# Kernel optimization log

Measured on AMD Instinct MI355X. Metric: run time of the kernel, lower is better.

The kernel has to match this reference:

```python
import jax, jax.numpy as jnp
import numpy as np

N_PER_TYPE = 32000
N = 3 * N_PER_TYPE          # 96000 nodes
E = N * 16                  # 1,536,000 edges
H, D = 4, 8                 # num_heads, out_dim per head; hidden = 32
IN_DIMS = [128, 64, 32]
NEG_SLOPE = 0.2


def setup_inputs() -> dict:
    key = jax.random.key(0)
    ks = jax.random.split(key, 16)
    inp = {}
    # per-type raw features
    inp['x0'] = jax.random.normal(ks[0], (N_PER_TYPE, IN_DIMS[0]), jnp.float32)
    inp['x1'] = jax.random.normal(ks[1], (N_PER_TYPE, IN_DIMS[1]), jnp.float32)
    inp['x2'] = jax.random.normal(ks[2], (N_PER_TYPE, IN_DIMS[2]), jnp.float32)
    # per-type linear params (fc_list), scaled like kaiming-ish init
    inp['W0'] = jax.random.normal(ks[3], (IN_DIMS[0], H * D), jnp.float32) / np.sqrt(IN_DIMS[0])
    inp['b0'] = jnp.zeros((H * D,), jnp.float32)
    inp['W1'] = jax.random.normal(ks[4], (IN_DIMS[1], H * D), jnp.float32) / np.sqrt(IN_DIMS[1])
    inp['b1'] = jnp.zeros((H * D,), jnp.float32)
    inp['W2'] = jax.random.normal(ks[5], (IN_DIMS[2], H * D), jnp.float32) / np.sqrt(IN_DIMS[2])
    inp['b2'] = jnp.zeros((H * D,), jnp.float32)
    # GAT attention vectors a_l, a_r per head
    inp['attn_l'] = jax.random.normal(ks[6], (H, D), jnp.float32) / np.sqrt(D)
    inp['attn_r'] = jax.random.normal(ks[7], (H, D), jnp.float32) / np.sqrt(D)
    # node types laid out in contiguous blocks -> fixed-size index sets
    inp['type_mask'] = jnp.repeat(jnp.arange(3, dtype=jnp.int32), N_PER_TYPE)
    inp['idx0'] = jnp.arange(0, N_PER_TYPE, dtype=jnp.int32)
    inp['idx1'] = jnp.arange(N_PER_TYPE, 2 * N_PER_TYPE, dtype=jnp.int32)
    inp['idx2'] = jnp.arange(2 * N_PER_TYPE, 3 * N_PER_TYPE, dtype=jnp.int32)
    # random edge list
    inp['src'] = jax.random.randint(ks[8], (E,), 0, N, jnp.int32)
    inp['dst'] = jax.random.randint(ks[9], (E,), 0, N, jnp.int32)
    return inp


def reference(x0, x1, x2, W0, b0, W1, b1, W2, b2, attn_l, attn_r,
              idx0, idx1, idx2, src, dst, type_mask):
    # ---- type-masked per-type linear embed scattered into dense buffer ----
    t = jnp.zeros((N, H * D), x0.dtype)
    t = t.at[idx0].set(x0 @ W0 + b0)
    t = t.at[idx1].set(x1 @ W1 + b1)
    t = t.at[idx2].set(x2 @ W2 + b2)
    # (feat_drop is identity in eval mode)
    h = t.reshape(N, H, D)
    # ---- multi-head GAT attention ----
    el = jnp.einsum('nhd,hd->nh', h, attn_l)   # [N,H]
    er = jnp.einsum('nhd,hd->nh', h, attn_r)   # [N,H]
    e = jax.nn.leaky_relu(el[src] + er[dst], NEG_SLOPE)  # [E,H]
    # segment softmax over incoming edges of each dst node
    m = jax.ops.segment_max(e, dst, num_segments=N)      # [N,H]
    m = jnp.where(jnp.isfinite(m), m, 0.0)               # guard isolated nodes
    ex = jnp.exp(e - m[dst])                             # [E,H]
    s = jax.ops.segment_sum(ex, dst, num_segments=N)     # [N,H]
    alpha = ex / (s[dst] + 1e-9)                         # [E,H]
    # message aggregation
    msg = alpha[:, :, None] * h[src]                     # [E,H,D]
    out = jax.ops.segment_sum(msg, dst, num_segments=N)  # [N,H,D]
    # concat heads + ELU (standard intermediate-layer GAT activation)
    return jax.nn.elu(out).reshape(N, H * D)
```

## Files before the change

kernel.cpp:

```cpp
#include <hip/hip_runtime.h>
#include <hip/hip_bf16.h>
#include <math.h>

#define N_PER_TYPE 32000
#define NN (3 * N_PER_TYPE)
#define EDGES (NN * 16)
#define NHEAD 4
#define HD 32
#define NEG 0.2f
#define BINS 256
#define NPB (NN / BINS)
#define TILES 256
#define TPE (EDGES / TILES)
#define MAXBIN 8192
#define NB_EMBED 1500

typedef __attribute__((ext_vector_type(8))) short bf16x8;
typedef __attribute__((ext_vector_type(4))) float f32x4;

__device__ __forceinline__ unsigned packbf(float a, float b) {
    __hip_bfloat162 t = __float22bfloat162_rn(make_float2(a, b));
    return *reinterpret_cast<unsigned*>(&t);
}

__global__ __launch_bounds__(256) void embed_p1_kernel(
    const float* __restrict__ x0, const float* __restrict__ x1, const float* __restrict__ x2,
    const float* __restrict__ W0, const float* __restrict__ b0,
    const float* __restrict__ W1, const float* __restrict__ b1,
    const float* __restrict__ W2, const float* __restrict__ b2,
    const float* __restrict__ attn_l, const float* __restrict__ attn_r,
    __hip_bfloat16* __restrict__ h16, float* __restrict__ el, float* __restrict__ er,
    const int* __restrict__ dst, int* __restrict__ counts)
{
    int blk = blockIdx.x;
    int tid = threadIdx.x;

    if (blk >= NB_EMBED) {
        __shared__ int hist[BINS];
        int tile = blk - NB_EMBED;
        for (int i = tid; i < BINS; i += 256) hist[i] = 0;
        __syncthreads();
        int e0 = tile * TPE;
        for (int t = e0 + tid; t < e0 + TPE; t += 256)
            atomicAdd(&hist[dst[t] / NPB], 1);
        __syncthreads();
        for (int i = tid; i < BINS; i += 256) counts[tile * BINS + i] = hist[i];
        return;
    }

    __shared__ unsigned Wb[2048];
    __shared__ float hepi[64][33];

    int type = blk / 500;
    int nb = blk % 500;

    const float* x; const float* W; const float* bia; int in_dim;
    if (type == 0)      { x = x0; W = W0; bia = b0; in_dim = 128; }
    else if (type == 1) { x = x1; W = W1; bia = b1; in_dim = 64; }
    else                { x = x2; W = W2; bia = b2; in_dim = 32; }
    int KS = in_dim >> 5;

    int ndw = KS << 9;
    for (int i = tid; i < ndw; i += 256) {
        int d = i & 3, l = (i >> 2) & 63, sn = i >> 8;
        int s = sn >> 1, n = sn & 1;
        int k = (s << 5) + ((l >> 4) << 3) + (d << 1);
        int col = (n << 4) + (l & 15);
        Wb[i] = packbf(W[k * 32 + col], W[(k + 1) * 32 + col]);
    }
    __syncthreads();

    int wave = tid >> 6, lane = tid & 63;
    int node_l0 = wave * 16 + (lane & 15);
    const float* xrow = x + (size_t)(nb * 64 + node_l0) * in_dim;
    int kg = lane >> 4;

    f32x4 acc0 = {0.f, 0.f, 0.f, 0.f};
    f32x4 acc1 = {0.f, 0.f, 0.f, 0.f};

    for (int s = 0; s < KS; ++s) {
        int k0 = (s << 5) + (kg << 3);
        float4 xa = *(const float4*)(xrow + k0);
        float4 xb = *(const float4*)(xrow + k0 + 4);
        union { unsigned u[4]; bf16x8 v; } a;
        a.u[0] = packbf(xa.x, xa.y);
        a.u[1] = packbf(xa.z, xa.w);
        a.u[2] = packbf(xb.x, xb.y);
        a.u[3] = packbf(xb.z, xb.w);
        bf16x8 bfr0 = *(const bf16x8*)&Wb[((s * 2 + 0) * 64 + lane) * 4];
        bf16x8 bfr1 = *(const bf16x8*)&Wb[((s * 2 + 1) * 64 + lane) * 4];
        acc0 = __builtin_amdgcn_mfma_f32_16x16x32_bf16(a.v, bfr0, acc0, 0, 0, 0);
        acc1 = __builtin_amdgcn_mfma_f32_16x16x32_bf16(a.v, bfr1, acc1, 0, 0, 0);
    }

    int hrow = wave * 16 + ((lane >> 4) << 2);
    int hcol = lane & 15;
    #pragma unroll
    for (int r = 0; r < 4; ++r) {
        hepi[hrow + r][hcol]      = acc0[r];
        hepi[hrow + r][hcol + 16] = acc1[r];
    }
    __syncthreads();

    int node_e = tid >> 2, head = tid & 3;
    int node = blk * 64 + node_e;
    float4 al = *(const float4*)(attn_l + head * 8);
    float4 al2 = *(const float4*)(attn_l + head * 8 + 4);
    float4 ar = *(const float4*)(attn_r + head * 8);
    float4 ar2 = *(const float4*)(attn_r + head * 8 + 4);
    float hv[8];
    #pragma unroll
    for (int i = 0; i < 8; ++i) hv[i] = hepi[node_e][head * 8 + i] + bia[head * 8 + i];

    float elv = hv[0]*al.x + hv[1]*al.y + hv[2]*al.z + hv[3]*al.w
              + hv[4]*al2.x + hv[5]*al2.y + hv[6]*al2.z + hv[7]*al2.w;
    float erv = hv[0]*ar.x + hv[1]*ar.y + hv[2]*ar.z + hv[3]*ar.w
              + hv[4]*ar2.x + hv[5]*ar2.y + hv[6]*ar2.z + hv[7]*ar2.w;
    el[node * NHEAD + head] = elv;
    er[node * NHEAD + head] = erv;

    uint4 o;
    o.x = packbf(hv[0], hv[1]);
    o.y = packbf(hv[2], hv[3]);
    o.z = packbf(hv[4], hv[5]);
    o.w = packbf(hv[6], hv[7]);
    *reinterpret_cast<uint4*>((unsigned short*)h16 + (size_t)node * HD + head * 8) = o;
}

__global__ __launch_bounds__(256) void colscan_kernel(const int* __restrict__ counts,
                                                      int* __restrict__ colscan,
                                                      int* __restrict__ total) {
    __shared__ int s[256];
    int b = blockIdx.x, t = threadIdx.x;
    int v = counts[t * BINS + b];
    s[t] = v;
    __syncthreads();
    #pragma unroll
    for (int off = 1; off < 256; off <<= 1) {
        int tv = (t >= off) ? s[t - off] : 0;
        __syncthreads();
        s[t] += tv;
        __syncthreads();
    }
    colscan[t * BINS + b] = s[t] - v;
    if (t == 255) total[b] = s[255];
}

__global__ __launch_bounds__(256) void bstart_kernel(const int* __restrict__ total,
                                                     int* __restrict__ bstart) {
    __shared__ int s[256];
    int t = threadIdx.x;
    int v = total[t];
    s[t] = v;
    __syncthreads();
    #pragma unroll
    for (int off = 1; off < 256; off <<= 1) {
        int tv = (t >= off) ? s[t - off] : 0;
        __syncthreads();
        s[t] += tv;
        __syncthreads();
    }
    bstart[t] = s[t] - v;
    if (t == 255) bstart[256] = s[255];
}

__global__ __launch_bounds__(1024) void reorder_kernel(
    const int* __restrict__ src, const int* __restrict__ dst,
    const int* __restrict__ colscan, const int* __restrict__ bstart,
    unsigned* __restrict__ rec2)
{
    __shared__ int hist[BINS];
    __shared__ int sscan[BINS];
    __shared__ int prefix[BINS];
    __shared__ int offg[BINS];
    __shared__ unsigned sorted[TPE];
    __shared__ unsigned char binof[TPE];

    int tile = blockIdx.x, tid = threadIdx.x;
    for (int i = tid; i < BINS; i += 1024) hist[i] = 0;
    __syncthreads();

    int e0 = tile * TPE;
    unsigned rv[6]; int rb[6]; int rk[6]; int ne = 0;
    for (int t = e0 + tid; t < e0 + TPE; t += 1024) {
        int d = dst[t];
        int bin = d / NPB;
        int dl = d - bin * NPB;
        rv[ne] = ((unsigned)src[t] << 9) | (unsigned)dl;
        rb[ne] = bin;
        rk[ne] = atomicAdd(&hist[bin], 1);
        ++ne;
    }
    __syncthreads();

    if (tid < BINS) sscan[tid] = hist[tid];
    __syncthreads();
    #pragma unroll
    for (int off = 1; off < BINS; off <<= 1) {
        int tv = 0;
        if (tid < BINS && tid >= off) tv = sscan[tid - off];
        __syncthreads();
        if (tid < BINS) sscan[tid] += tv;
        __syncthreads();
    }
    if (tid < BINS) {
        int ex = sscan[tid] - hist[tid];
        prefix[tid] = ex;
        offg[tid] = bstart[tid] + colscan[tile * BINS + tid] - ex;
    }
    __syncthreads();

    #pragma unroll
    for (int q = 0; q < 6; ++q) if (q < ne) {
        int p = prefix[rb[q]] + rk[q];
        sorted[p] = rv[q];
        binof[p] = (unsigned char)rb[q];
    }
    __syncthreads();

    for (int j = tid; j < TPE; j += 1024) {
        int bin = binof[j];
        rec2[offg[bin] + j] = sorted[j];
    }
}

__global__ __launch_bounds__(1024) void placeagg_kernel(
    const unsigned* __restrict__ rec2, const int* __restrict__ bstart,
    const float* __restrict__ el, const float* __restrict__ er,
    const __hip_bfloat16* __restrict__ h16, float* __restrict__ out)
{
    __shared__ int ncnt[NPB];
    __shared__ int noff[NPB];
    __shared__ int sc[512];
    __shared__ int ldscsr[MAXBIN];

    int k = blockIdx.x, tid = threadIdx.x;
    int bs = bstart[k];
    int be = bstart[k + 1];
    int cnt = be - bs;
    if (cnt > MAXBIN) cnt = MAXBIN;

    for (int i = tid; i < NPB; i += 1024) ncnt[i] = 0;
    __syncthreads();

    unsigned rsrc[8]; int rdl[8]; int rk8[8]; int ne = 0;
    for (int t = bs + tid; t < bs + cnt; t += 1024) {
        unsigned r = rec2[t];
        int dl = (int)(r & 511u);
        rsrc[ne] = r >> 9;
        rdl[ne] = dl;
        rk8[ne] = atomicAdd(&ncnt[dl], 1);
        ++ne;
    }
    __syncthreads();

    int v = 0;
    if (tid < 512) { v = (tid < NPB) ? ncnt[tid] : 0; sc[tid] = v; }
    __syncthreads();
    #pragma unroll
    for (int off = 1; off < 512; off <<= 1) {
        int tv = 0;
        if (tid < 512 && tid >= off) tv = sc[tid - off];
        __syncthreads();
        if (tid < 512) sc[tid] += tv;
        __syncthreads();
    }
    if (tid < NPB) noff[tid] = sc[tid] - v;
    __syncthreads();

    #pragma unroll
    for (int q = 0; q < 8; ++q) if (q < ne)
        ldscsr[noff[rdl[q]] + rk8[q]] = (int)rsrc[q];
    __syncthreads();

    const unsigned* hp = (const unsigned*)h16;
    int grp = tid >> 4;
    int j = tid & 15;
    int head = j >> 2;
    int hh = j & 3;

    #pragma unroll
    for (int rnd = 0; rnd < 6; ++rnd) {
        int dl = rnd * 64 + grp;
        if (dl < NPB) {
            int s0 = noff[dl];
            int len = ncnt[dl];
            int node = k * NPB + dl;
            float er_s = er[node * NHEAD + hh];
            float acc0 = 0.f, acc1 = 0.f, den = 0.f;

            for (int base = 0; base < len; base += 16) {
                int c16 = len - base; if (c16 > 16) c16 = 16;
                int svl = (j < c16) ? ldscsr[s0 + base + j] : 0;
                for (int c = 0; c < c16; c += 4) {
                    int se = c + (j >> 2);
                    int sv_s = __shfl(svl, se, 16);
                    float xs = el[sv_s * NHEAD + hh] + er_s;
                    xs = fmaxf(xs, NEG * xs);
                    float exf = (se < c16) ? __expf(xs) : 0.0f;
                    #pragma unroll
                    for (int i = 0; i < 4; ++i) {
                        int sv = __shfl(svl, c + i, 16);
                        float ex = __shfl(exf, (i << 2) + head, 16);
                        unsigned p = hp[sv * 16 + j];
                        den += ex;
                        acc0 = fmaf(ex, __uint_as_float(p << 16),         acc0);
                        acc1 = fmaf(ex, __uint_as_float(p & 0xffff0000u), acc1);
                    }
                }
            }
            den += 1e-9f;
            float v0 = acc0 / den, v1 = acc1 / den;
            v0 = v0 > 0.f ? v0 : expm1f(v0);
            v1 = v1 > 0.f ? v1 : expm1f(v1);
            *reinterpret_cast<float2*>(out + node * HD + (j << 1)) = make_float2(v0, v1);
        }
    }
}

extern "C" void kernel_launch(void* const* d_in, const int* in_sizes, int n_in,
                              void* d_out, int out_size, void* d_ws, size_t ws_size,
                              hipStream_t stream) {
    const float* x0 = (const float*)d_in[0];
    const float* x1 = (const float*)d_in[1];
    const float* x2 = (const float*)d_in[2];
    const float* W0 = (const float*)d_in[3];
    const float* b0 = (const float*)d_in[4];
    const float* W1 = (const float*)d_in[5];
    const float* b1 = (const float*)d_in[6];
    const float* W2 = (const float*)d_in[7];
    const float* b2 = (const float*)d_in[8];
    const float* attn_l = (const float*)d_in[9];
    const float* attn_r = (const float*)d_in[10];
    const int* src = (const int*)d_in[15];
    const int* dst = (const int*)d_in[16];
    float* out = (float*)d_out;

    __hip_bfloat16* h16 = (__hip_bfloat16*)d_ws;
    float* el = (float*)(h16 + NN * HD);
    float* er = el + NN * NHEAD;
    int* counts  = (int*)(er + NN * NHEAD);
    int* colscan = counts + TILES * BINS;
    int* total   = colscan + TILES * BINS;
    int* bstart  = total + BINS;
    unsigned* rec2 = (unsigned*)(bstart + 260);

    embed_p1_kernel<<<NB_EMBED + TILES, 256, 0, stream>>>(
        x0, x1, x2, W0, b0, W1, b1, W2, b2,
        attn_l, attn_r, h16, el, er, dst, counts);
    colscan_kernel<<<BINS, 256, 0, stream>>>(counts, colscan, total);
    bstart_kernel<<<1, 256, 0, stream>>>(total, bstart);
    reorder_kernel<<<TILES, 1024, 0, stream>>>(src, dst, colscan, bstart, rec2);
    placeagg_kernel<<<BINS, 1024, 0, stream>>>(rec2, bstart, el, er, h16, out);
}
```

Measured before the change: 64.90 us.

## Fold bin-start scan into consumers, double reorder tiles, unroll exp computation

Removes the single-block bstart kernel launch by recomputing the bin-total prefix scan redundantly inside each reorder and placeagg block. Doubles the number of reorder tiles so each block handles fewer edges and more blocks run in parallel. In the aggregation loop, all four exp batches are computed before the accumulation loop rather than interleaved with it. The cost is redundant per-block scans and extra barriers, and the embed kernel's histogram part now has twice as many tile blocks.

```diff
diff --git a/kernel.cpp b/kernel.cpp
--- a/kernel.cpp
+++ b/kernel.cpp
@@ -10,7 +10,7 @@
 #define NEG 0.2f
 #define BINS 256
 #define NPB (NN / BINS)
-#define TILES 256
+#define TILES 512
 #define TPE (EDGES / TILES)
 #define MAXBIN 8192
 #define NB_EMBED 1500
@@ -127,61 +127,55 @@
     *reinterpret_cast<uint4*>((unsigned short*)h16 + (size_t)node * HD + head * 8) = o;
 }
 
-__global__ __launch_bounds__(256) void colscan_kernel(const int* __restrict__ counts,
+__global__ __launch_bounds__(512) void colscan_kernel(const int* __restrict__ counts,
                                                       int* __restrict__ colscan,
                                                       int* __restrict__ total) {
-    __shared__ int s[256];
+    __shared__ int s[TILES];
     int b = blockIdx.x, t = threadIdx.x;
     int v = counts[t * BINS + b];
     s[t] = v;
     __syncthreads();
     #pragma unroll
-    for (int off = 1; off < 256; off <<= 1) {
+    for (int off = 1; off < TILES; off <<= 1) {
         int tv = (t >= off) ? s[t - off] : 0;
         __syncthreads();
         s[t] += tv;
         __syncthreads();
     }
     colscan[t * BINS + b] = s[t] - v;
-    if (t == 255) total[b] = s[255];
-}
-
-__global__ __launch_bounds__(256) void bstart_kernel(const int* __restrict__ total,
-                                                     int* __restrict__ bstart) {
-    __shared__ int s[256];
-    int t = threadIdx.x;
-    int v = total[t];
-    s[t] = v;
-    __syncthreads();
-    #pragma unroll
-    for (int off = 1; off < 256; off <<= 1) {
-        int tv = (t >= off) ? s[t - off] : 0;
-        __syncthreads();
-        s[t] += tv;
-        __syncthreads();
-    }
-    bstart[t] = s[t] - v;
-    if (t == 255) bstart[256] = s[255];
+    if (t == TILES - 1) total[b] = s[TILES - 1];
 }
 
 __global__ __launch_bounds__(1024) void reorder_kernel(
     const int* __restrict__ src, const int* __restrict__ dst,
-    const int* __restrict__ colscan, const int* __restrict__ bstart,
+    const int* __restrict__ colscan, const int* __restrict__ total,
     unsigned* __restrict__ rec2)
 {
     __shared__ int hist[BINS];
     __shared__ int sscan[BINS];
-    __shared__ int prefix[BINS];
+    __shared__ int bst[BINS];
     __shared__ int offg[BINS];
     __shared__ unsigned sorted[TPE];
     __shared__ unsigned char binof[TPE];
 
     int tile = blockIdx.x, tid = threadIdx.x;
     for (int i = tid; i < BINS; i += 1024) hist[i] = 0;
+    int bv = 0;
+    if (tid < BINS) { bv = total[tid]; bst[tid] = bv; }
+    __syncthreads();
+    #pragma unroll
+    for (int off = 1; off < BINS; off <<= 1) {
+        int tv = 0;
+        if (tid < BINS && tid >= off) tv = bst[tid - off];
+        __syncthreads();
+        if (tid < BINS) bst[tid] += tv;
+        __syncthreads();
+    }
+    if (tid < BINS) bst[tid] -= bv;
     __syncthreads();
 
     int e0 = tile * TPE;
-    unsigned rv[6]; int rb[6]; int rk[6]; int ne = 0;
+    unsigned rv[3]; int rb[3]; int rk[3]; int ne = 0;
     for (int t = e0 + tid; t < e0 + TPE; t += 1024) {
         int d = dst[t];
         int bin = d / NPB;
@@ -205,14 +199,14 @@
     }
     if (tid < BINS) {
         int ex = sscan[tid] - hist[tid];
-        prefix[tid] = ex;
-        offg[tid] = bstart[tid] + colscan[tile * BINS + tid] - ex;
-    }
-    __syncthreads();
-
-    #pragma unroll
-    for (int q = 0; q < 6; ++q) if (q < ne) {
-        int p = prefix[rb[q]] + rk[q];
+        offg[tid] = bst[tid] + colscan[tile * BINS + tid] - ex;
+        sscan[tid] = ex;
+    }
+    __syncthreads();
+
+    #pragma unroll
+    for (int q = 0; q < 3; ++q) if (q < ne) {
+        int p = sscan[rb[q]] + rk[q];
         sorted[p] = rv[q];
         binof[p] = (unsigned char)rb[q];
     }
@@ -225,7 +219,7 @@
 }
 
 __global__ __launch_bounds__(1024) void placeagg_kernel(
-    const unsigned* __restrict__ rec2, const int* __restrict__ bstart,
+    const unsigned* __restrict__ rec2, const int* __restrict__ total,
     const float* __restrict__ el, const float* __restrict__ er,
     const __hip_bfloat16* __restrict__ h16, float* __restrict__ out)
 {
@@ -235,10 +229,22 @@
     __shared__ int ldscsr[MAXBIN];
 
     int k = blockIdx.x, tid = threadIdx.x;
-    int bs = bstart[k];
-    int be = bstart[k + 1];
-    int cnt = be - bs;
+
+    int v512 = 0;
+    if (tid < 512) { v512 = (tid < BINS) ? total[tid] : 0; sc[tid] = v512; }
+    __syncthreads();
+    #pragma unroll
+    for (int off = 1; off < 512; off <<= 1) {
+        int tv = 0;
+        if (tid < 512 && tid >= off) tv = sc[tid - off];
+        __syncthreads();
+        if (tid < 512) sc[tid] += tv;
+        __syncthreads();
+    }
+    int bs = sc[k] - total[k];
+    int cnt = total[k];
     if (cnt > MAXBIN) cnt = MAXBIN;
+    __syncthreads();
 
     for (int i = tid; i < NPB; i += 1024) ncnt[i] = 0;
     __syncthreads();
@@ -290,18 +296,23 @@
             float acc0 = 0.f, acc1 = 0.f, den = 0.f;
 
             for (int base = 0; base < len; base += 16) {
-                int c16 = len - base; if (c16 > 16) c16 = 16;
-                int svl = (j < c16) ? ldscsr[s0 + base + j] : 0;
-                for (int c = 0; c < c16; c += 4) {
-                    int se = c + (j >> 2);
+                int rem = len - base;
+                int svl = (j < rem) ? ldscsr[s0 + base + j] : 0;
+                float exf[4];
+                #pragma unroll
+                for (int c4 = 0; c4 < 4; ++c4) {
+                    int se = (c4 << 2) + (j >> 2);
                     int sv_s = __shfl(svl, se, 16);
                     float xs = el[sv_s * NHEAD + hh] + er_s;
                     xs = fmaxf(xs, NEG * xs);
-                    float exf = (se < c16) ? __expf(xs) : 0.0f;
+                    exf[c4] = (se < rem) ? __expf(xs) : 0.0f;
+                }
+                #pragma unroll
+                for (int c4 = 0; c4 < 4; ++c4) {
                     #pragma unroll
                     for (int i = 0; i < 4; ++i) {
-                        int sv = __shfl(svl, c + i, 16);
-                        float ex = __shfl(exf, (i << 2) + head, 16);
+                        int sv = __shfl(svl, (c4 << 2) + i, 16);
+                        float ex = __shfl(exf[c4], (i << 2) + head, 16);
                         unsigned p = hp[sv * 16 + j];
                         den += ex;
                         acc0 = fmaf(ex, __uint_as_float(p << 16),         acc0);
@@ -342,14 +353,12 @@
     int* counts  = (int*)(er + NN * NHEAD);
     int* colscan = counts + TILES * BINS;
     int* total   = colscan + TILES * BINS;
-    int* bstart  = total + BINS;
-    unsigned* rec2 = (unsigned*)(bstart + 260);
+    unsigned* rec2 = (unsigned*)(total + 512);
 
     embed_p1_kernel<<<NB_EMBED + TILES, 256, 0, stream>>>(
         x0, x1, x2, W0, b0, W1, b1, W2, b2,
         attn_l, attn_r, h16, el, er, dst, counts);
-    colscan_kernel<<<BINS, 256, 0, stream>>>(counts, colscan, total);
-    bstart_kernel<<<1, 256, 0, stream>>>(total, bstart);
-    reorder_kernel<<<TILES, 1024, 0, stream>>>(src, dst, colscan, bstart, rec2);
-    placeagg_kernel<<<BINS, 1024, 0, stream>>>(rec2, bstart, el, er, h16, out);
-}
+    colscan_kernel<<<BINS, TILES, 0, stream>>>(counts, colscan, total);
+    reorder_kernel<<<TILES, 1024, 0, stream>>>(src, dst, colscan, total, rec2);
+    placeagg_kernel<<<BINS, 1024, 0, stream>>>(rec2, total, el, er, h16, out);
+}
```

Result: no change. 63.75 us (-1.8%).
